# Performance work log

Measured on AMD Instinct MI355X. Metric: run time of the kernel, lower is better.

The kernel has to match this reference:

```python
import jax, jax.numpy as jnp
import numpy as np

HIDDEN = 1024
ARC = 500
BATCH = 16
SEQ = 512


def setup_inputs() -> dict:
    key = jax.random.key(0)
    ks = jax.random.split(key, 12)
    s_h = 1.0 / np.sqrt(HIDDEN)
    s_a = 1.0 / np.sqrt(ARC)
    return {
        "hidden_states": jax.random.normal(ks[0], (BATCH, SEQ, HIDDEN), dtype=jnp.float32),
        # head MLP: Linear(hidden->arc), ReLU, (Dropout eval=identity), Linear(arc->arc)
        "w1h": jax.random.uniform(ks[1], (ARC, HIDDEN), jnp.float32, -s_h, s_h),
        "b1h": jax.random.uniform(ks[2], (ARC,), jnp.float32, -s_h, s_h),
        "w2h": jax.random.uniform(ks[3], (ARC, ARC), jnp.float32, -s_a, s_a),
        "b2h": jax.random.uniform(ks[4], (ARC,), jnp.float32, -s_a, s_a),
        # dep MLP
        "w1d": jax.random.uniform(ks[5], (ARC, HIDDEN), jnp.float32, -s_h, s_h),
        "b1d": jax.random.uniform(ks[6], (ARC,), jnp.float32, -s_h, s_h),
        "w2d": jax.random.uniform(ks[7], (ARC, ARC), jnp.float32, -s_a, s_a),
        "b2d": jax.random.uniform(ks[8], (ARC,), jnp.float32, -s_a, s_a),
        # nn.Bilinear(arc, arc, 1, bias=True): weight [1, arc, arc], bias [1]
        "Wb": jax.random.uniform(ks[9], (ARC, ARC), jnp.float32, -s_a, s_a),
        "bb": jax.random.uniform(ks[10], (1,), jnp.float32, -s_a, s_a),
    }


def reference(hidden_states, w1h, b1h, w2h, b2h, w1d, b1d, w2d, b2d, Wb, bb):
    # MLPs (dropout is identity at inference)
    head = jnp.maximum(hidden_states @ w1h.T + b1h, 0.0) @ w2h.T + b2h  # [B,S,A]
    dep = jnp.maximum(hidden_states @ w1d.T + b1d, 0.0) @ w2d.T + b2d  # [B,S,A]
    # seq_len <= 512 already; chunked bilinear == two GEMMs:
    # scores[b,i,j] = head[b,i] @ Wb @ dep[b,j] + bb
    headW = head @ Wb  # [B,S,A]
    arc_scores = jnp.einsum("bia,bja->bij", headW, dep) + bb[0]  # [B,S,S]
    return arc_scores
```

## Files before the change

### kernel.cpp

```cpp
#include <hip/hip_runtime.h>
#include <hip/hip_bf16.h>


#define HIDDEN 1024
#define ARC 500
#define AP 512
#define ROWS 8192

typedef __attribute__((ext_vector_type(4))) float f32x4;
typedef __attribute__((ext_vector_type(8))) short short8;

static __device__ __forceinline__ ushort f2bf(float f) {
  union { float f; unsigned u; } v; v.f = f;
  unsigned r = v.u + 0x7fffu + ((v.u >> 16) & 1u);
  return (ushort)(r >> 16);
}

__global__ void k_prep_all(const float* __restrict__ w1h, const float* __restrict__ b1h,
                           const float* __restrict__ w1d, const float* __restrict__ b1d,
                           const float* __restrict__ w2h, const float* __restrict__ b2h,
                           const float* __restrict__ w2d, const float* __restrict__ b2d,
                           const float* __restrict__ Wb, const float4* __restrict__ hs,
                           ushort* __restrict__ W1, ushort* __restrict__ WbT,
                           ushort* __restrict__ w2hT, ushort* __restrict__ W2,
                           float* __restrict__ b1c, ushort* __restrict__ hs_bf) {
  const int bid = blockIdx.x;
  const int tid = threadIdx.x;
  if (bid < 4096) {
    int idx = bid * 256 + tid;
    int n = idx >> 10, k = idx & 1023;
    float v = 0.f;
    if (n < ARC) v = w1h[(size_t)n * HIDDEN + k];
    else if (n >= AP && n < AP + ARC) v = w1d[(size_t)(n - AP) * HIDDEN + k];
    W1[idx] = f2bf(v);
  } else if (bid < 5120) {
    int idx = (bid - 4096) * 256 + tid;
    int a = idx >> 9, j = idx & 511;
    float v = (a < ARC && j < ARC) ? Wb[(size_t)j * ARC + a] : 0.f;
    WbT[idx] = f2bf(v);
  } else if (bid < 6144) {
    int idx = (bid - 5120) * 256 + tid;
    int k = idx >> 9, j = idx & 511;
    float v = 0.f;
    if (j < ARC) {
      if (k < ARC) v = w2h[(size_t)j * ARC + k];
      else if (k == 511) v = b2h[j];
    }
    w2hT[idx] = f2bf(v);
  } else if (bid < 7168) {
    int idx = (bid - 6144) * 256 + tid;
    int n = idx >> 9, k = idx & 511;
    float v = 0.f;
    if (n < ARC) {
      if (k < ARC) v = w2d[(size_t)n * ARC + k];
      else if (k == 511) v = b2d[n];
    }
    W2[idx] = f2bf(v);
  } else if (bid < 7172) {
    int i = (bid - 7168) * 256 + tid;
    float v = 0.f;
    if (i < ARC) v = b1h[i];
    else if (i == 511 || i == 1023) v = 1.f;
    else if (i >= AP && i < AP + ARC) v = b1d[i - AP];
    b1c[i] = v;
  } else {
    const int n4 = ROWS * HIDDEN / 4;
    int i = (bid - 7172) * 256 + tid;
    for (; i < n4; i += 2048 * 256) {
      float4 v = hs[i];
      ushort4 o;
      o.x = f2bf(v.x); o.y = f2bf(v.y); o.z = f2bf(v.z); o.w = f2bf(v.w);
      *(ushort4*)(hs_bf + (size_t)i * 4) = o;
    }
  }
}

template <int BN>
__device__ __forceinline__ void gemm_body(
    const ushort* __restrict__ A, const ushort* __restrict__ B,
    const float* __restrict__ bias, int bias_mode,
    void* __restrict__ C, int out_bf16, int relu,
    int lda, int ldb, int ldc, int K, int tm, int tn, ushort* lds) {
  constexpr int WC = BN / 2;
  constexpr int NFR = WC / 16;
  constexpr int BUFSZ = 4096 + BN * 32;

  const int t = threadIdx.x;
  const int w = t >> 6;
  const int l = t & 63;
  const int wr = w >> 1, wc = w & 1;

  f32x4 acc[4][NFR];
#pragma unroll
  for (int m = 0; m < 4; ++m)
#pragma unroll
    for (int n = 0; n < NFR; ++n) acc[m][n] = f32x4{0.f, 0.f, 0.f, 0.f};

  const int srow = w * 16 + (l >> 2);
  const int scol = (((l & 3) ^ ((l >> 3) & 3))) * 8;
  const ushort* ag = A + (size_t)(tm + srow) * lda + scol;
  const ushort* bg = B + (size_t)(tn + srow) * ldb + scol;
  const int lofs = w * 512;

  const int fr = l & 15, fh = l >> 4;
  const int swz = (fr >> 1) & 3;
  const int fAo = (wr * 64 + fr) * 32 + (fh ^ swz) * 8;
  const int fBo = (wc * WC + fr) * 32 + (fh ^ swz) * 8;

  auto stage = [&](int kt, ushort* buf) {
#pragma unroll
    for (int c = 0; c < 2; ++c)
      __builtin_amdgcn_global_load_lds(
          (const __attribute__((address_space(1))) void*)(ag + (size_t)c * 64 * lda + kt),
          (__attribute__((address_space(3))) void*)(buf + lofs + c * 2048), 16, 0, 0);
#pragma unroll
    for (int c = 0; c < BN / 64; ++c)
      __builtin_amdgcn_global_load_lds(
          (const __attribute__((address_space(1))) void*)(bg + (size_t)c * 64 * ldb + kt),
          (__attribute__((address_space(3))) void*)(buf + 4096 + lofs + c * 2048), 16, 0, 0);
  };
  auto compute = [&](const ushort* buf) {
    short8 af[4], bf[NFR];
#pragma unroll
    for (int m = 0; m < 4; ++m) af[m] = *(const short8*)(buf + fAo + m * 16 * 32);
#pragma unroll
    for (int n = 0; n < NFR; ++n) bf[n] = *(const short8*)(buf + 4096 + fBo + n * 16 * 32);
#pragma unroll
    for (int m = 0; m < 4; ++m)
#pragma unroll
      for (int n = 0; n < NFR; ++n)
        acc[m][n] = __builtin_amdgcn_mfma_f32_16x16x32_bf16(af[m], bf[n], acc[m][n], 0, 0, 0);
  };

  const int nt = K >> 5;
  stage(0, lds);
  stage(32, lds + BUFSZ);
  int cs = 0, ps = 2;
  for (int ti = 0; ti < nt; ++ti) {
    if (ti + 1 < nt) {
      if constexpr (BN == 128) asm volatile("s_waitcnt vmcnt(4)" ::: "memory");
      else                     asm volatile("s_waitcnt vmcnt(3)" ::: "memory");
    } else {
      asm volatile("s_waitcnt vmcnt(0)" ::: "memory");
    }
    __builtin_amdgcn_s_barrier();
    __builtin_amdgcn_sched_barrier(0);
    if (ti + 2 < nt) stage((ti + 2) << 5, lds + ps * BUFSZ);
    compute(lds + cs * BUFSZ);
    cs = (cs == 2) ? 0 : cs + 1;
    ps = (ps == 2) ? 0 : ps + 1;
  }

  const int cr = fh * 4;
  const float bscal = (bias_mode == 2) ? bias[0] : 0.f;
#pragma unroll
  for (int m = 0; m < 4; ++m) {
#pragma unroll
    for (int n = 0; n < NFR; ++n) {
      const int col = tn + wc * WC + n * 16 + fr;
      const float bv = (bias_mode == 1) ? bias[col] : bscal;
#pragma unroll
      for (int j = 0; j < 4; ++j) {
        const int row = tm + wr * 64 + m * 16 + cr + j;
        float v = acc[m][n][j] + bv;
        if (relu) v = fmaxf(v, 0.f);
        if (out_bf16)
          ((ushort*)C)[(size_t)row * ldc + col] = f2bf(v);
        else
          ((float*)C)[(size_t)row * ldc + col] = v;
      }
    }
  }
}

__global__ __launch_bounds__(256)
void k_g1mt(const ushort* __restrict__ hs_bf, const ushort* __restrict__ W1,
            const float* __restrict__ b1c, ushort* __restrict__ t1,
            const ushort* __restrict__ WbT, const ushort* __restrict__ w2hT,
            ushort* __restrict__ MTb) {
  __shared__ ushort lds[3 * 8192];
  const int flat = blockIdx.y * 8 + blockIdx.x;
  const int f2 = (flat & 7) * 66 + (flat >> 3);
  const int by = f2 >> 3, bx = f2 & 7;
  if (by < 64) {
    gemm_body<128>(hs_bf, W1, b1c, 1, t1, 1, 1,
                   HIDDEN, HIDDEN, 1024, HIDDEN, by * 128, bx * 128, lds);
  } else {
    const int idx = (by - 64) * 8 + bx;
    gemm_body<128>(WbT, w2hT, nullptr, 0, MTb, 1, 0,
                   AP, AP, AP, AP, (idx >> 2) * 128, (idx & 3) * 128, lds);
  }
}

template <int BN>
__global__ __launch_bounds__(256)
void k_gemm_rt(const ushort* __restrict__ A, const ushort* __restrict__ B,
               const float* __restrict__ bias, int bias_mode,
               void* __restrict__ C, int out_bf16, int relu,
               int lda, int ldb, int ldc, int K,
               long aBS, long bBS, long cBS) {
  __shared__ ushort lds[3 * (4096 + BN * 32)];
  const int gx = gridDim.x, gy = gridDim.y;
  const int gxy = gx * gy;
  const int nwg = gxy * gridDim.z;
  const int flat = (blockIdx.z * gy + blockIdx.y) * gx + blockIdx.x;
  const int q = nwg >> 3;
  const int f2 = (flat & 7) * q + (flat >> 3);
  const int bz = f2 / gxy;
  const int rm = f2 - bz * gxy;
  const int by = rm / gx;
  const int bx = rm - by * gx;

  const ushort* Az = A + (size_t)aBS * bz;
  const ushort* Bz = B + (size_t)bBS * bz;
  void* Cz = out_bf16 ? (void*)((ushort*)C + (size_t)cBS * bz)
                      : (void*)((float*)C + (size_t)cBS * bz);
  gemm_body<BN>(Az, Bz, bias, bias_mode, Cz, out_bf16, relu,
                lda, ldb, ldc, K, by * 128, bx * BN, lds);
}

extern "C" void kernel_launch(void* const* d_in, const int* in_sizes, int n_in,
                              void* d_out, int out_size, void* d_ws, size_t ws_size,
                              hipStream_t stream) {
  const float* hs  = (const float*)d_in[0];
  const float* w1h = (const float*)d_in[1];
  const float* b1h = (const float*)d_in[2];
  const float* w2h = (const float*)d_in[3];
  const float* b2h = (const float*)d_in[4];
  const float* w1d = (const float*)d_in[5];
  const float* b1d = (const float*)d_in[6];
  const float* w2d = (const float*)d_in[7];
  const float* b2d = (const float*)d_in[8];
  const float* Wb  = (const float*)d_in[9];
  const float* bb  = (const float*)d_in[10];

  char* ws = (char*)d_ws;
  ushort* hs_bf = (ushort*)(ws + 0);
  ushort* W1    = (ushort*)(ws + 16777216);
  ushort* WbT   = (ushort*)(ws + 18874368);
  ushort* w2hT  = (ushort*)(ws + 19398656);
  ushort* MT    = (ushort*)(ws + 19922944);
  ushort* W2    = (ushort*)(ws + 20447232);
  ushort* t1    = (ushort*)(ws + 20971520);
  ushort* hw    = (ushort*)(ws + 37748736);
  float*  b1c   = (float*)(ws + 54525952);
  float*  out   = (float*)d_out;

  k_prep_all<<<9220, 256, 0, stream>>>(w1h, b1h, w1d, b1d, w2h, b2h, w2d, b2d,
                                       Wb, (const float4*)hs,
                                       W1, WbT, w2hT, W2, b1c, hs_bf);

  k_g1mt<<<dim3(8, 66), 256, 0, stream>>>(hs_bf, W1, b1c, t1, WbT, w2hT, MT);

  k_gemm_rt<128><<<dim3(4, 64, 2), 256, 0, stream>>>(
      t1, MT, nullptr, 0, hw, 1, 0, 1024, AP, AP, AP,
      AP, (long)AP * AP, (long)ROWS * AP);

  k_gemm_rt<64><<<dim3(8, 4, 16), 256, 0, stream>>>(
      hw, hw + (size_t)ROWS * AP, bb, 2, out, 0, 0, AP, AP, 512, AP,
      (long)512 * AP, (long)512 * AP, (long)512 * 512);
}
```

Baseline: 163.3 us.

## Fold both MLP second layers and bilinear into one dep-side matrix, deepen pipeline

Reassociates the bilinear score: the head-side second layer and Wb are folded together with the dep-side second layer into a single 512x512 matrix S. Only one 8192x512 GEMM (hidden-dep times S) is then needed, and the final batched GEMM reads the hidden-head activations from t1 directly. This replaces the earlier two activation GEMMs (head@MT and dep@W2). The GEMM main loop also moves from triple to quadruple LDS buffering with prefetch distance 3, adjusts the vmcnt waits to match, and raises wave priority around the MFMA block. The cost is more LDS per block, which may lower occupancy, and an extra small serial GEMM launch.

```diff
diff --git a/kernel.cpp b/kernel.cpp
--- a/kernel.cpp
+++ b/kernel.cpp
@@ -22,7 +22,7 @@
                            const float* __restrict__ w2d, const float* __restrict__ b2d,
                            const float* __restrict__ Wb, const float4* __restrict__ hs,
                            ushort* __restrict__ W1, ushort* __restrict__ WbT,
-                           ushort* __restrict__ w2hT, ushort* __restrict__ W2,
+                           ushort* __restrict__ w2hT, ushort* __restrict__ W2T,
                            float* __restrict__ b1c, ushort* __restrict__ hs_bf) {
   const int bid = blockIdx.x;
   const int tid = threadIdx.x;
@@ -49,13 +49,13 @@
     w2hT[idx] = f2bf(v);
   } else if (bid < 7168) {
     int idx = (bid - 6144) * 256 + tid;
-    int n = idx >> 9, k = idx & 511;
-    float v = 0.f;
-    if (n < ARC) {
-      if (k < ARC) v = w2d[(size_t)n * ARC + k];
-      else if (k == 511) v = b2d[n];
-    }
-    W2[idx] = f2bf(v);
+    int m = idx >> 9, a = idx & 511;
+    float v = 0.f;
+    if (a < ARC) {
+      if (m < ARC) v = w2d[(size_t)a * ARC + m];
+      else if (m == 511) v = b2d[a];
+    }
+    W2T[idx] = f2bf(v);
   } else if (bid < 7172) {
     int i = (bid - 7168) * 256 + tid;
     float v = 0.f;
@@ -135,9 +135,13 @@
   const int nt = K >> 5;
   stage(0, lds);
   stage(32, lds + BUFSZ);
-  int cs = 0, ps = 2;
+  stage(64, lds + 2 * BUFSZ);
+  int cs = 0, ps = 3;
   for (int ti = 0; ti < nt; ++ti) {
-    if (ti + 1 < nt) {
+    if (ti < nt - 2) {
+      if constexpr (BN == 128) asm volatile("s_waitcnt vmcnt(8)" ::: "memory");
+      else                     asm volatile("s_waitcnt vmcnt(6)" ::: "memory");
+    } else if (ti == nt - 2) {
       if constexpr (BN == 128) asm volatile("s_waitcnt vmcnt(4)" ::: "memory");
       else                     asm volatile("s_waitcnt vmcnt(3)" ::: "memory");
     } else {
@@ -145,10 +149,12 @@
     }
     __builtin_amdgcn_s_barrier();
     __builtin_amdgcn_sched_barrier(0);
-    if (ti + 2 < nt) stage((ti + 2) << 5, lds + ps * BUFSZ);
+    if (ti + 3 < nt) stage((ti + 3) << 5, lds + ps * BUFSZ);
+    __builtin_amdgcn_s_setprio(1);
     compute(lds + cs * BUFSZ);
-    cs = (cs == 2) ? 0 : cs + 1;
-    ps = (ps == 2) ? 0 : ps + 1;
+    __builtin_amdgcn_s_setprio(0);
+    cs = (cs + 1) & 3;
+    ps = (ps + 1) & 3;
   }
 
   const int cr = fh * 4;
@@ -176,9 +182,9 @@
 __global__ __launch_bounds__(256)
 void k_g1mt(const ushort* __restrict__ hs_bf, const ushort* __restrict__ W1,
             const float* __restrict__ b1c, ushort* __restrict__ t1,
-            const ushort* __restrict__ WbT, const ushort* __restrict__ w2hT,
-            ushort* __restrict__ MTb) {
-  __shared__ ushort lds[3 * 8192];
+            const ushort* __restrict__ w2hT, const ushort* __restrict__ WbT,
+            ushort* __restrict__ MTT) {
+  __shared__ ushort lds[4 * 8192];
   const int flat = blockIdx.y * 8 + blockIdx.x;
   const int f2 = (flat & 7) * 66 + (flat >> 3);
   const int by = f2 >> 3, bx = f2 & 7;
@@ -187,7 +193,7 @@
                    HIDDEN, HIDDEN, 1024, HIDDEN, by * 128, bx * 128, lds);
   } else {
     const int idx = (by - 64) * 8 + bx;
-    gemm_body<128>(WbT, w2hT, nullptr, 0, MTb, 1, 0,
+    gemm_body<128>(w2hT, WbT, nullptr, 0, MTT, 1, 0,
                    AP, AP, AP, AP, (idx >> 2) * 128, (idx & 3) * 128, lds);
   }
 }
@@ -199,7 +205,7 @@
                void* __restrict__ C, int out_bf16, int relu,
                int lda, int ldb, int ldc, int K,
                long aBS, long bBS, long cBS) {
-  __shared__ ushort lds[3 * (4096 + BN * 32)];
+  __shared__ ushort lds[4 * (4096 + BN * 32)];
   const int gx = gridDim.x, gy = gridDim.y;
   const int gxy = gx * gy;
   const int nwg = gxy * gridDim.z;
@@ -239,24 +245,27 @@
   ushort* W1    = (ushort*)(ws + 16777216);
   ushort* WbT   = (ushort*)(ws + 18874368);
   ushort* w2hT  = (ushort*)(ws + 19398656);
-  ushort* MT    = (ushort*)(ws + 19922944);
-  ushort* W2    = (ushort*)(ws + 20447232);
+  ushort* MTT   = (ushort*)(ws + 19922944);
+  ushort* W2T   = (ushort*)(ws + 20447232);
   ushort* t1    = (ushort*)(ws + 20971520);
-  ushort* hw    = (ushort*)(ws + 37748736);
+  ushort* dep2  = (ushort*)(ws + 37748736);
+  ushort* S     = (ushort*)(ws + 46137344);
   float*  b1c   = (float*)(ws + 54525952);
   float*  out   = (float*)d_out;
 
   k_prep_all<<<9220, 256, 0, stream>>>(w1h, b1h, w1d, b1d, w2h, b2h, w2d, b2d,
                                        Wb, (const float4*)hs,
-                                       W1, WbT, w2hT, W2, b1c, hs_bf);
-
-  k_g1mt<<<dim3(8, 66), 256, 0, stream>>>(hs_bf, W1, b1c, t1, WbT, w2hT, MT);
-
-  k_gemm_rt<128><<<dim3(4, 64, 2), 256, 0, stream>>>(
-      t1, MT, nullptr, 0, hw, 1, 0, 1024, AP, AP, AP,
-      AP, (long)AP * AP, (long)ROWS * AP);
+                                       W1, WbT, w2hT, W2T, b1c, hs_bf);
+
+  k_g1mt<<<dim3(8, 66), 256, 0, stream>>>(hs_bf, W1, b1c, t1, w2hT, WbT, MTT);
+
+  k_gemm_rt<128><<<dim3(4, 4, 1), 256, 0, stream>>>(
+      MTT, W2T, nullptr, 0, S, 1, 0, AP, AP, AP, AP, 0, 0, 0);
+
+  k_gemm_rt<128><<<dim3(4, 64, 1), 256, 0, stream>>>(
+      t1 + AP, S, nullptr, 0, dep2, 1, 0, 1024, AP, AP, AP, 0, 0, 0);
 
   k_gemm_rt<64><<<dim3(8, 4, 16), 256, 0, stream>>>(
-      hw, hw + (size_t)ROWS * AP, bb, 2, out, 0, 0, AP, AP, 512, AP,
-      (long)512 * AP, (long)512 * AP, (long)512 * 512);
-}
+      t1, dep2, bb, 2, out, 0, 0, 1024, AP, 512, AP,
+      (long)512 * 1024, (long)512 * AP, (long)512 * 512);
+}
```

Result: slower. 177.0 us (+8.4%).
